# Optimization experiments

Hardware: AMD Instinct MI355X
Metric: run time of the kernel (lower is better)

Reference implementation:

```python
import jax, jax.numpy as jnp
import numpy as np
from jax import lax

V, E, H, MLP, NCLS = 50000, 100, 100, 300, 3
B, T, C = 256, 128, 255


def _lstm_dir(x, Wih, Whh, bih, bhh, reverse):
    # x: [T, B, E]; PyTorch gate order i, f, g, o
    Bsz = x.shape[1]
    h0 = jnp.zeros((Bsz, H), x.dtype)
    c0 = jnp.zeros((Bsz, H), x.dtype)

    def step(carry, xt):
        h, c = carry
        gates = xt @ Wih.T + h @ Whh.T + (bih + bhh)  # [B, 4H]
        i, f, g, o = jnp.split(gates, 4, axis=-1)
        c = jax.nn.sigmoid(f) * c + jax.nn.sigmoid(i) * jnp.tanh(g)
        h = jax.nn.sigmoid(o) * jnp.tanh(c)
        return (h, c), h

    _, hs = lax.scan(step, (h0, c0), x, reverse=reverse)
    return hs  # [T, B, H]


def setup_inputs() -> dict:
    key = jax.random.key(0)
    ks = jax.random.split(key, 16)
    s_e = 1.0 / np.sqrt(H)
    inp = {
        "x": jax.random.randint(ks[0], (B, T), 0, V),
        "paths": jax.random.randint(ks[1], (B, C, 3), 0, T),
        "emb": jax.random.normal(ks[2], (V, E), jnp.float32),
        "Wih_f": jax.random.uniform(ks[3], (4 * H, E), jnp.float32, -s_e, s_e),
        "Whh_f": jax.random.uniform(ks[4], (4 * H, H), jnp.float32, -s_e, s_e),
        "bih_f": jax.random.uniform(ks[5], (4 * H,), jnp.float32, -s_e, s_e),
        "bhh_f": jax.random.uniform(ks[6], (4 * H,), jnp.float32, -s_e, s_e),
        "Wih_b": jax.random.uniform(ks[7], (4 * H, E), jnp.float32, -s_e, s_e),
        "Whh_b": jax.random.uniform(ks[8], (4 * H, H), jnp.float32, -s_e, s_e),
        "bih_b": jax.random.uniform(ks[9], (4 * H,), jnp.float32, -s_e, s_e),
        "bhh_b": jax.random.uniform(ks[10], (4 * H,), jnp.float32, -s_e, s_e),
        "W1": jax.random.normal(ks[11], (6 * H, MLP), jnp.float32) * 0.05,
        "b1": jnp.zeros((MLP,), jnp.float32),
        "W2": jax.random.normal(ks[12], (MLP, NCLS), jnp.float32) * 0.05,
        "b2": jnp.zeros((NCLS,), jnp.float32),
    }
    return inp


def reference(x, paths, emb, Wih_f, Whh_f, bih_f, bhh_f, Wih_b, Whh_b, bih_b, bhh_b, W1, b1, W2, b2):
    # embedding lookup (dropout is eval-mode identity)
    xe = emb[x]                      # [B, T, E]
    xe = jnp.transpose(xe, (1, 0, 2))  # [T, B, E] (seq-major like packed LSTM)
    hf = _lstm_dir(xe, Wih_f, Whh_f, bih_f, bhh_f, reverse=False)
    hb = _lstm_dir(xe, Wih_b, Whh_b, bih_b, bhh_b, reverse=True)
    h = jnp.concatenate([hf, hb], axis=-1)        # [T, B, 2H]
    hbt = jnp.transpose(h, (1, 0, 2))             # [B, T, 2H]
    # gather 3 positions per configuration; index -1 -> zero vector
    idx = jnp.clip(paths, 0, T - 1)               # [B, C, 3]
    g = hbt[jnp.arange(hbt.shape[0])[:, None, None], idx]  # [B, C, 3, 2H]
    g = jnp.where((paths >= 0)[..., None], g, 0.0)
    mlp_in = g.reshape(-1, 6 * H)                 # [B*C, 600]
    hdn = jnp.tanh(mlp_in @ W1 + b1)
    return jax.nn.softmax(hdn @ W2 + b2, axis=-1)  # [B*C, 3]
```

## Files before the change

kernel.cpp:

```cpp
#include <hip/hip_runtime.h>

typedef unsigned short u16;
typedef short short8 __attribute__((ext_vector_type(8)));
typedef float f32x4 __attribute__((ext_vector_type(4)));

__device__ __forceinline__ u16 f2b(float x){
  union{float f; unsigned u;} v; v.f = x;
  unsigned r = (v.u + 0x7FFFu + ((v.u >> 16) & 1u)) >> 16;
  return (u16)r;
}
__device__ __forceinline__ float b2f(u16 h){
  union{unsigned u; float f;} v; v.u = ((unsigned)h) << 16; return v.f;
}
__device__ __forceinline__ float sigm(float x){ return 1.0f/(1.0f + __expf(-x)); }
__device__ __forceinline__ float tanh_f(float x){ return 1.0f - 2.0f/(1.0f + __expf(2.0f*x)); }

__global__ void prep_kernel(const int* __restrict__ x, const float* __restrict__ emb,
   const float* __restrict__ Wih_f, const float* __restrict__ Whh_f,
   const float* __restrict__ bih_f, const float* __restrict__ bhh_f,
   const float* __restrict__ Wih_b, const float* __restrict__ Whh_b,
   const float* __restrict__ bih_b, const float* __restrict__ bhh_b,
   const float* __restrict__ W1,
   u16* __restrict__ xe, u16* __restrict__ wc, float* __restrict__ biasC,
   float* __restrict__ whhT, u16* __restrict__ w1b, u16* __restrict__ hbt)
{
  int id = blockIdx.x*256 + threadIdx.x;
  const int N0 = 32768*128;
  const int N1 = 832*128;
  const int N2 = 800;
  const int N3 = 80000;
  const int N4 = 672*320;
  const int N5 = 32768*24;
  if (id < N0){
    int p = id >> 7, k = id & 127;
    float v = 0.f;
    if (k < 100) v = emb[x[p]*100 + k];
    xe[id] = f2b(v);
    return;
  }
  id -= N0;
  if (id < N1){
    int n = id >> 7, k = id & 127;
    float v = 0.f;
    if (k < 100){
      if (n < 400) v = Wih_f[n*100+k];
      else if (n < 800) v = Wih_b[(n-400)*100+k];
    }
    wc[id] = f2b(v);
    return;
  }
  id -= N1;
  if (id < N2){
    biasC[id] = (id < 400) ? (bih_f[id]+bhh_f[id]) : (bih_b[id-400]+bhh_b[id-400]);
    return;
  }
  id -= N2;
  if (id < N3){
    int d = id / 40000; int rem = id - d*40000; int k = rem / 400; int j = rem - k*400;
    const float* W = d ? Whh_b : Whh_f;
    whhT[id] = W[j*100 + k];
    return;
  }
  id -= N3;
  if (id < N4){
    int k = id / 320; int n = id - k*320;
    int seg = k / 224; int wwk = k - seg*224;
    float v = 0.f;
    if (n < 300 && wwk < 200) v = W1[(seg*200 + wwk)*300 + n];
    w1b[n*672 + k] = f2b(v);
    return;
  }
  id -= N4;
  if (id < N5){
    int p = id / 24; int k = id - p*24;
    hbt[p*224 + 200 + k] = 0;
  }
}

__global__ __launch_bounds__(256) void gemm1_kernel(const u16* __restrict__ xe,
    const u16* __restrict__ wc, const float* __restrict__ biasC, u16* __restrict__ inp)
{
  __shared__ __align__(16) u16 As[64*136];
  __shared__ __align__(16) u16 Bs[64*136];
  const int m0 = blockIdx.x*64, n0 = blockIdx.y*64;
  const int tid = threadIdx.x;
  #pragma unroll
  for (int i=0;i<4;i++){
    int f = i*256 + tid;
    int row = f >> 4, c8 = f & 15;
    *(uint4*)&As[row*136 + c8*8] = *(const uint4*)&xe[(m0+row)*128 + c8*8];
    *(uint4*)&Bs[row*136 + c8*8] = *(const uint4*)&wc[(n0+row)*128 + c8*8];
  }
  __syncthreads();
  const int w = tid >> 6, lane = tid & 63, col = lane & 15, quad = lane >> 4;
  f32x4 acc[4];
  #pragma unroll
  for (int nt=0;nt<4;nt++) acc[nt] = (f32x4){0.f,0.f,0.f,0.f};
  #pragma unroll
  for (int kc=0;kc<4;kc++){
    short8 af = *(const short8*)&As[(w*16+col)*136 + kc*32 + quad*8];
    #pragma unroll
    for (int nt=0;nt<4;nt++){
      short8 bfrag = *(const short8*)&Bs[(nt*16+col)*136 + kc*32 + quad*8];
      acc[nt] = __builtin_amdgcn_mfma_f32_16x16x32_bf16(af, bfrag, acc[nt], 0, 0, 0);
    }
  }
  #pragma unroll
  for (int nt=0;nt<4;nt++){
    int n = n0 + nt*16 + col;
    if (n < 800){
      float bs = biasC[n];
      int dir = (n >= 400) ? 1 : 0;
      int j = n - dir*400;
      #pragma unroll
      for (int r=0;r<4;r++){
        int m = m0 + w*16 + quad*4 + r;
        inp[(dir*32768 + m)*400 + j] = f2b(acc[nt][r] + bs);
      }
    }
  }
}

__global__ __launch_bounds__(448, 4) void lstm_kernel(const u16* __restrict__ inp,
    const float* __restrict__ whhT, u16* __restrict__ hbt)
{
  const int cid = blockIdx.x;
  const int b = cid & 255, dir = cid >> 8;
  const int jj = threadIdx.x;
  __shared__ __align__(16) float hs[104];
  __shared__ float act[400];
  float whh[100];
  if (jj < 400){
    const float* wp = whhT + dir*40000 + jj;
    #pragma unroll
    for (int k=0;k<100;k++) whh[k] = wp[k*400];
  }
  if (jj < 104) hs[jj] = 0.f;
  float c = 0.f;
  const u16* ip = inp + (dir*32768 + b*128)*400;
  u16* hp = hbt + b*128*224;
  __syncthreads();
  for (int step=0; step<128; step++){
    int t = dir ? (127-step) : step;
    if (jj < 400){
      float pre = b2f(ip[t*400 + jj]);
      const float4* h4 = (const float4*)hs;
      float a0=0.f,a1=0.f,a2=0.f,a3=0.f;
      #pragma unroll
      for (int kk=0;kk<25;kk++){
        float4 hv = h4[kk];
        a0 = fmaf(whh[4*kk+0], hv.x, a0);
        a1 = fmaf(whh[4*kk+1], hv.y, a1);
        a2 = fmaf(whh[4*kk+2], hv.z, a2);
        a3 = fmaf(whh[4*kk+3], hv.w, a3);
      }
      float xg = pre + ((a0+a1)+(a2+a3));
      act[jj] = (jj >= 200 && jj < 300) ? tanh_f(xg) : sigm(xg);
    }
    __syncthreads();
    if (jj < 100){
      float ig = act[jj], fg = act[100+jj], gg = act[200+jj], og = act[300+jj];
      c = fg*c + ig*gg;
      float hk = og * tanh_f(c);
      hs[jj] = hk;
      hp[t*224 + dir*100 + jj] = f2b(hk);
    }
    __syncthreads();
  }
}

__global__ __launch_bounds__(512) void mlp_kernel(const u16* __restrict__ hbt,
    const u16* __restrict__ w1b, const int* __restrict__ paths,
    const float* __restrict__ b1, const float* __restrict__ W2,
    const float* __restrict__ b2, float* __restrict__ out)
{
  __shared__ __align__(16) u16 As[128*40];
  __shared__ __align__(16) u16 Bs[320*40];
  const int m0 = blockIdx.x*128;
  const int tid = threadIdx.x;
  const int arow = tid >> 2, ac8 = tid & 3;
  const int am = m0 + arow;
  const int ab = am / 255;
  const int w = tid >> 6, lane = tid & 63, col = lane & 15, quad = lane >> 4;
  f32x4 acc[20];
  #pragma unroll
  for (int nt=0;nt<20;nt++) acc[nt] = (f32x4){0.f,0.f,0.f,0.f};
  for (int kc=0;kc<21;kc++){
    __syncthreads();
    for (int f = tid; f < 1280; f += 512){
      int br = f >> 2, bc = f & 3;
      *(uint4*)&Bs[br*40 + bc*8] = *(const uint4*)&w1b[br*672 + kc*32 + bc*8];
    }
    int seg = (kc >= 14) ? 2 : (kc >= 7 ? 1 : 0);
    int ko = kc - seg*7;
    int it = paths[am*3 + seg];
    uint4 v = make_uint4(0u,0u,0u,0u);
    if (it >= 0){
      int t = it > 127 ? 127 : it;
      v = *(const uint4*)&hbt[(ab*128 + t)*224 + ko*32 + ac8*8];
    }
    *(uint4*)&As[arow*40 + ac8*8] = v;
    __syncthreads();
    short8 af = *(const short8*)&As[(w*16+col)*40 + quad*8];
    #pragma unroll
    for (int nt=0;nt<20;nt++){
      short8 bfrag = *(const short8*)&Bs[(nt*16+col)*40 + quad*8];
      acc[nt] = __builtin_amdgcn_mfma_f32_16x16x32_bf16(af, bfrag, acc[nt], 0, 0, 0);
    }
  }
  float pz[4][3];
  #pragma unroll
  for (int r=0;r<4;r++){ pz[r][0]=0.f; pz[r][1]=0.f; pz[r][2]=0.f; }
  #pragma unroll
  for (int nt=0;nt<20;nt++){
    int n = nt*16 + col;
    if (n < 300){
      float bb = b1[n];
      float w20 = W2[n*3+0], w21 = W2[n*3+1], w22 = W2[n*3+2];
      #pragma unroll
      for (int r=0;r<4;r++){
        float hdn = tanh_f(acc[nt][r] + bb);
        pz[r][0] = fmaf(hdn, w20, pz[r][0]);
        pz[r][1] = fmaf(hdn, w21, pz[r][1]);
        pz[r][2] = fmaf(hdn, w22, pz[r][2]);
      }
    }
  }
  #pragma unroll
  for (int off=1; off<16; off<<=1){
    #pragma unroll
    for (int r=0;r<4;r++){
      pz[r][0] += __shfl_xor(pz[r][0], off, 64);
      pz[r][1] += __shfl_xor(pz[r][1], off, 64);
      pz[r][2] += __shfl_xor(pz[r][2], off, 64);
    }
  }
  float c0 = b2[0], c1 = b2[1], c2 = b2[2];
  #pragma unroll
  for (int r=0;r<4;r++){
    float z0 = pz[r][0]+c0, z1 = pz[r][1]+c1, z2 = pz[r][2]+c2;
    float mx = fmaxf(z0, fmaxf(z1, z2));
    float e0 = __expf(z0-mx), e1 = __expf(z1-mx), e2 = __expf(z2-mx);
    float inv = 1.0f/(e0+e1+e2);
    if (col < 3){
      float pv = (col==0 ? e0 : (col==1 ? e1 : e2)) * inv;
      out[(m0 + w*16 + quad*4 + r)*3 + col] = pv;
    }
  }
}

extern "C" void kernel_launch(void* const* d_in, const int* in_sizes, int n_in,
                              void* d_out, int out_size, void* d_ws, size_t ws_size,
                              hipStream_t stream)
{
  const int*   x     = (const int*)  d_in[0];
  const int*   paths = (const int*)  d_in[1];
  const float* emb   = (const float*)d_in[2];
  const float* Wih_f = (const float*)d_in[3];
  const float* Whh_f = (const float*)d_in[4];
  const float* bih_f = (const float*)d_in[5];
  const float* bhh_f = (const float*)d_in[6];
  const float* Wih_b = (const float*)d_in[7];
  const float* Whh_b = (const float*)d_in[8];
  const float* bih_b = (const float*)d_in[9];
  const float* bhh_b = (const float*)d_in[10];
  const float* W1    = (const float*)d_in[11];
  const float* b1    = (const float*)d_in[12];
  const float* W2    = (const float*)d_in[13];
  const float* b2    = (const float*)d_in[14];
  float* out = (float*)d_out;

  char* ws = (char*)d_ws;
  u16*   xe    = (u16*)  (ws + 0);
  u16*   wc    = (u16*)  (ws + 8388608);
  float* biasC = (float*)(ws + 8601600);
  float* whhT  = (float*)(ws + 8604800);
  u16*   w1b   = (u16*)  (ws + 8924800);
  u16*   inp   = (u16*)  (ws + 9354880);
  u16*   hbt   = (u16*)  (ws + 61783680);

  const int prep_total = 32768*128 + 832*128 + 800 + 80000 + 672*320 + 32768*24;
  prep_kernel<<<(prep_total + 255)/256, 256, 0, stream>>>(
      x, emb, Wih_f, Whh_f, bih_f, bhh_f, Wih_b, Whh_b, bih_b, bhh_b, W1,
      xe, wc, biasC, whhT, w1b, hbt);
  gemm1_kernel<<<dim3(512, 13), 256, 0, stream>>>(xe, wc, biasC, inp);
  lstm_kernel<<<512, 448, 0, stream>>>(inp, whhT, hbt);
  mlp_kernel<<<510, 512, 0, stream>>>(hbt, w1b, paths, b1, W2, b2, out);
}
```

Before: 364.4 us.

## Split LSTM recurrent dot product across two threads per gate

The recurrent matvec in the LSTM kernel now uses two threads per gate row. Each thread holds 50 weights instead of 100, and the two halves are combined with a lane shuffle. The Whh weights are repacked into an interleaved layout to match, and the per-step pointer arithmetic for t is replaced with incrementing pointers. This halves the serial FMA chain per step on the latency-bound recurrence and lowers register pressure. In exchange the block grows to 832 threads, each step adds a shuffle, and only half the threads do the activation.

```diff
diff --git a/kernel.cpp b/kernel.cpp
--- a/kernel.cpp
+++ b/kernel.cpp
@@ -22,7 +22,7 @@
    const float* __restrict__ bih_b, const float* __restrict__ bhh_b,
    const float* __restrict__ W1,
    u16* __restrict__ xe, u16* __restrict__ wc, float* __restrict__ biasC,
-   float* __restrict__ whhT, u16* __restrict__ w1b, u16* __restrict__ hbt)
+   float* __restrict__ whhP, u16* __restrict__ w1b, u16* __restrict__ hbt)
 {
   int id = blockIdx.x*256 + threadIdx.x;
   const int N0 = 32768*128;
@@ -56,9 +56,10 @@
   }
   id -= N2;
   if (id < N3){
-    int d = id / 40000; int rem = id - d*40000; int k = rem / 400; int j = rem - k*400;
+    int d = id / 40000; int rem = id - d*40000; int kk = rem / 800; int p = rem - kk*800;
+    int j = p >> 1, half = p & 1;
     const float* W = d ? Whh_b : Whh_f;
-    whhT[id] = W[j*100 + k];
+    whhP[id] = W[j*100 + half*50 + kk];
     return;
   }
   id -= N3;
@@ -121,50 +122,60 @@
   }
 }
 
-__global__ __launch_bounds__(448, 4) void lstm_kernel(const u16* __restrict__ inp,
-    const float* __restrict__ whhT, u16* __restrict__ hbt)
+__global__ __launch_bounds__(832, 7) void lstm_kernel(const u16* __restrict__ inp,
+    const float* __restrict__ whhP, u16* __restrict__ hbt)
 {
   const int cid = blockIdx.x;
   const int b = cid & 255, dir = cid >> 8;
-  const int jj = threadIdx.x;
+  const int tid = threadIdx.x;
+  const int j = tid >> 1, half = tid & 1;
   __shared__ __align__(16) float hs[104];
   __shared__ float act[400];
-  float whh[100];
-  if (jj < 400){
-    const float* wp = whhT + dir*40000 + jj;
+  float whh[50];
+  if (tid < 800){
+    const float* wp = whhP + dir*40000 + tid;
     #pragma unroll
-    for (int k=0;k<100;k++) whh[k] = wp[k*400];
-  }
-  if (jj < 104) hs[jj] = 0.f;
+    for (int k=0;k<50;k++) whh[k] = wp[k*800];
+  }
+  if (tid < 104) hs[tid] = 0.f;
   float c = 0.f;
-  const u16* ip = inp + (dir*32768 + b*128)*400;
-  u16* hp = hbt + b*128*224;
+  const u16* ipt = inp + (dir*32768 + b*128)*400 + (dir ? 127*400 : 0);
+  u16* hpt = hbt + b*128*224 + (dir ? 127*224 : 0) + dir*100 + tid;
+  const int dIp = dir ? -400 : 400;
+  const int dHp = dir ? -224 : 224;
   __syncthreads();
   for (int step=0; step<128; step++){
-    int t = dir ? (127-step) : step;
-    if (jj < 400){
-      float pre = b2f(ip[t*400 + jj]);
-      const float4* h4 = (const float4*)hs;
+    if (tid < 800){
+      const float2* h2 = (const float2*)(hs + half*50);
       float a0=0.f,a1=0.f,a2=0.f,a3=0.f;
       #pragma unroll
-      for (int kk=0;kk<25;kk++){
-        float4 hv = h4[kk];
-        a0 = fmaf(whh[4*kk+0], hv.x, a0);
-        a1 = fmaf(whh[4*kk+1], hv.y, a1);
-        a2 = fmaf(whh[4*kk+2], hv.z, a2);
-        a3 = fmaf(whh[4*kk+3], hv.w, a3);
+      for (int kk=0;kk<12;kk++){
+        float2 u = h2[2*kk], v = h2[2*kk+1];
+        a0 = fmaf(whh[4*kk+0], u.x, a0);
+        a1 = fmaf(whh[4*kk+1], u.y, a1);
+        a2 = fmaf(whh[4*kk+2], v.x, a2);
+        a3 = fmaf(whh[4*kk+3], v.y, a3);
       }
-      float xg = pre + ((a0+a1)+(a2+a3));
-      act[jj] = (jj >= 200 && jj < 300) ? tanh_f(xg) : sigm(xg);
+      { float2 u = h2[24];
+        a0 = fmaf(whh[48], u.x, a0);
+        a1 = fmaf(whh[49], u.y, a1); }
+      float part = (a0+a2)+(a1+a3);
+      part += __shfl_xor(part, 1, 64);
+      if (half == 0){
+        float xg = b2f(ipt[j]) + part;
+        act[j] = (j >= 200 && j < 300) ? tanh_f(xg) : sigm(xg);
+      }
     }
     __syncthreads();
-    if (jj < 100){
-      float ig = act[jj], fg = act[100+jj], gg = act[200+jj], og = act[300+jj];
+    if (tid < 100){
+      float ig = act[tid], fg = act[100+tid], gg = act[200+tid], og = act[300+tid];
       c = fg*c + ig*gg;
       float hk = og * tanh_f(c);
-      hs[jj] = hk;
-      hp[t*224 + dir*100 + jj] = f2b(hk);
-    }
+      hs[tid] = hk;
+      *hpt = f2b(hk);
+      hpt += dHp;
+    }
+    ipt += dIp;
     __syncthreads();
   }
 }
@@ -274,7 +285,7 @@
   u16*   xe    = (u16*)  (ws + 0);
   u16*   wc    = (u16*)  (ws + 8388608);
   float* biasC = (float*)(ws + 8601600);
-  float* whhT  = (float*)(ws + 8604800);
+  float* whhP  = (float*)(ws + 8604800);
   u16*   w1b   = (u16*)  (ws + 8924800);
   u16*   inp   = (u16*)  (ws + 9354880);
   u16*   hbt   = (u16*)  (ws + 61783680);
@@ -282,8 +293,8 @@
   const int prep_total = 32768*128 + 832*128 + 800 + 80000 + 672*320 + 32768*24;
   prep_kernel<<<(prep_total + 255)/256, 256, 0, stream>>>(
       x, emb, Wih_f, Whh_f, bih_f, bhh_f, Wih_b, Whh_b, bih_b, bhh_b, W1,
-      xe, wc, biasC, whhT, w1b, hbt);
+      xe, wc, biasC, whhP, w1b, hbt);
   gemm1_kernel<<<dim3(512, 13), 256, 0, stream>>>(xe, wc, biasC, inp);
-  lstm_kernel<<<512, 448, 0, stream>>>(inp, whhT, hbt);
+  lstm_kernel<<<512, 832, 0, stream>>>(inp, whhP, hbt);
   mlp_kernel<<<510, 512, 0, stream>>>(hbt, w1b, paths, b1, W2, b2, out);
 }
```

After: 529.0 us. 1.45x slower.

## Move LSTM recurrence to bf16 MFMA with split hi/lo precision, batching 8 sequences per block

Applied to the files above, without the earlier changes.

The recurrent h@Whh product moves from per-thread fp32 FMA over register-held weights to bf16 MFMA instructions. Weights and hidden state are each split into hi and lo bf16 parts (three MFMAs per chunk) to keep close to fp32 accuracy. Each block now handles 8 batch sequences of one direction (64 blocks instead of 512), and a dedicated warp prefetches the next step's input gates into double-buffered LDS. The prep kernel is reworked to emit the weights in MFMA fragment layout. The aim is more work per recurrent step and less per-step serial latency, at the cost of using only 64 blocks and relying on the split-bf16 scheme for accuracy.

```diff
diff --git a/kernel.cpp b/kernel.cpp
--- a/kernel.cpp
+++ b/kernel.cpp
@@ -22,13 +22,13 @@
    const float* __restrict__ bih_b, const float* __restrict__ bhh_b,
    const float* __restrict__ W1,
    u16* __restrict__ xe, u16* __restrict__ wc, float* __restrict__ biasC,
-   float* __restrict__ whhT, u16* __restrict__ w1b, u16* __restrict__ hbt)
+   u16* __restrict__ whhF, u16* __restrict__ w1b, u16* __restrict__ hbt)
 {
   int id = blockIdx.x*256 + threadIdx.x;
   const int N0 = 32768*128;
   const int N1 = 832*128;
   const int N2 = 800;
-  const int N3 = 80000;
+  const int N3 = 229376;
   const int N4 = 672*320;
   const int N5 = 32768*24;
   if (id < N0){
@@ -56,9 +56,24 @@
   }
   id -= N2;
   if (id < N3){
-    int d = id / 40000; int rem = id - d*40000; int k = rem / 400; int j = rem - k*400;
-    const float* W = d ? Whh_b : Whh_f;
-    whhT[id] = W[j*100 + k];
+    int dir = id / 114688; int r = id - dir*114688;
+    int tau = r >> 12;
+    int r2 = r & 4095;
+    int kc = r2 >> 10; int r3 = r2 & 1023;
+    int s  = r3 >> 9;  int r4 = r3 & 511;
+    int l  = r4 >> 3;  int e  = r4 & 7;
+    int g  = tau / 7;
+    int j  = (tau - g*7)*16 + (l & 15);
+    int kk = kc*32 + (l >> 4)*8 + e;
+    float v = 0.f;
+    if (j < 100 && kk < 100){
+      const float* W = dir ? Whh_b : Whh_f;
+      v = W[(g*100 + j)*100 + kk];
+    }
+    u16 hi = f2b(v);
+    u16 outv = hi;
+    if (s){ float lor = v - b2f(hi); outv = f2b(lor); }
+    whhF[id] = outv;
     return;
   }
   id -= N3;
@@ -121,49 +136,113 @@
   }
 }
 
-__global__ __launch_bounds__(448, 4) void lstm_kernel(const u16* __restrict__ inp,
-    const float* __restrict__ whhT, u16* __restrict__ hbt)
-{
-  const int cid = blockIdx.x;
-  const int b = cid & 255, dir = cid >> 8;
-  const int jj = threadIdx.x;
-  __shared__ __align__(16) float hs[104];
-  __shared__ float act[400];
-  float whh[100];
-  if (jj < 400){
-    const float* wp = whhT + dir*40000 + jj;
-    #pragma unroll
-    for (int k=0;k<100;k++) whh[k] = wp[k*400];
-  }
-  if (jj < 104) hs[jj] = 0.f;
-  float c = 0.f;
-  const u16* ip = inp + (dir*32768 + b*128)*400;
-  u16* hp = hbt + b*128*224;
+__global__ __launch_bounds__(512, 2) void lstm_kernel(const u16* __restrict__ inp,
+    const u16* __restrict__ whhF, u16* __restrict__ hbt)
+{
+  __shared__ __align__(16) u16 hhk[2][2][16][16][8];
+  __shared__ __align__(16) u16 inp_s[2][8][400];
+  const int beta = blockIdx.x;
+  const int dir = beta >> 5, b0 = (beta & 31) * 8;
+  const int tid = threadIdx.x;
+  const int w = tid >> 6, lane = tid & 63, col = lane & 15, q = lane >> 4;
+
+  for (int i = tid; i < 1024; i += 512) ((uint4*)hhk)[i] = make_uint4(0u,0u,0u,0u);
+
+  short8 wf[4][4][2];
+  f32x4 acc[4];
+  float cst[2]; cst[0] = 0.f; cst[1] = 0.f;
+  if (w < 7){
+    const u16* wp = whhF + (size_t)dir*114688;
+    #pragma unroll
+    for (int gi=0; gi<4; gi++)
+      #pragma unroll
+      for (int kc=0; kc<4; kc++)
+        #pragma unroll
+        for (int s=0; s<2; s++)
+          wf[gi][kc][s] = *(const short8*)&wp[(7*gi + w)*4096 + kc*1024 + s*512 + lane*8];
+  }
+  if (w == 7){
+    const int t0 = dir ? 127 : 0;
+    #pragma unroll
+    for (int i=0;i<7;i++){
+      int v = i*64 + lane;
+      if (v < 400){
+        int ch = v/50, off = v - ch*50;
+        const u16* gp = inp + ((size_t)(dir*32768 + (b0+ch)*128 + t0))*400 + off*8;
+        *(uint4*)&inp_s[0][ch][off*8] = *(const uint4*)gp;
+      }
+    }
+  }
   __syncthreads();
+
+  const int jl = 16*w + col;
+  const bool jv = (w < 7) && (jl < 100);
+  const int qq = q & 1;
+
   for (int step=0; step<128; step++){
-    int t = dir ? (127-step) : step;
-    if (jj < 400){
-      float pre = b2f(ip[t*400 + jj]);
-      const float4* h4 = (const float4*)hs;
-      float a0=0.f,a1=0.f,a2=0.f,a3=0.f;
-      #pragma unroll
-      for (int kk=0;kk<25;kk++){
-        float4 hv = h4[kk];
-        a0 = fmaf(whh[4*kk+0], hv.x, a0);
-        a1 = fmaf(whh[4*kk+1], hv.y, a1);
-        a2 = fmaf(whh[4*kk+2], hv.z, a2);
-        a3 = fmaf(whh[4*kk+3], hv.w, a3);
-      }
-      float xg = pre + ((a0+a1)+(a2+a3));
-      act[jj] = (jj >= 200 && jj < 300) ? tanh_f(xg) : sigm(xg);
-    }
-    __syncthreads();
-    if (jj < 100){
-      float ig = act[jj], fg = act[100+jj], gg = act[200+jj], og = act[300+jj];
-      c = fg*c + ig*gg;
-      float hk = og * tanh_f(c);
-      hs[jj] = hk;
-      hp[t*224 + dir*100 + jj] = f2b(hk);
+    const int t = dir ? 127-step : step;
+    const int par = step & 1;
+    if (w < 7){
+      short8 ah[4], al[4];
+      #pragma unroll
+      for (int kc=0; kc<4; kc++){
+        ah[kc] = *(const short8*)&hhk[par][0][kc*4+q][col][0];
+        al[kc] = *(const short8*)&hhk[par][1][kc*4+q][col][0];
+      }
+      #pragma unroll
+      for (int gi=0; gi<4; gi++){
+        f32x4 a = (f32x4){0.f,0.f,0.f,0.f};
+        #pragma unroll
+        for (int kc=0; kc<4; kc++){
+          a = __builtin_amdgcn_mfma_f32_16x16x32_bf16(ah[kc], wf[gi][kc][0], a, 0, 0, 0);
+          a = __builtin_amdgcn_mfma_f32_16x16x32_bf16(al[kc], wf[gi][kc][0], a, 0, 0, 0);
+          a = __builtin_amdgcn_mfma_f32_16x16x32_bf16(ah[kc], wf[gi][kc][1], a, 0, 0, 0);
+        }
+        acc[gi] = a;
+      }
+    }
+    if (w == 7 && step < 127){
+      int tn = dir ? 127-(step+1) : step+1;
+      #pragma unroll
+      for (int i=0;i<7;i++){
+        int v = i*64 + lane;
+        if (v < 400){
+          int ch = v/50, off = v - ch*50;
+          const u16* gp = inp + ((size_t)(dir*32768 + (b0+ch)*128 + tn))*400 + off*8;
+          *(uint4*)&inp_s[(step+1)&1][ch][off*8] = *(const uint4*)gp;
+        }
+      }
+    }
+    if (w < 7){
+      #pragma unroll
+      for (int u=0; u<2; u++){
+        float p0 = __shfl(acc[0][2+u], (lane+32)&63);
+        float p1 = __shfl(acc[1][2+u], (lane+32)&63);
+        float p2 = __shfl(acc[2][2+u], (lane+32)&63);
+        float p3 = __shfl(acc[3][2+u], (lane+32)&63);
+        float gI = (q < 2) ? acc[0][u] : p0;
+        float gF = (q < 2) ? acc[1][u] : p1;
+        float gG = (q < 2) ? acc[2][u] : p2;
+        float gO = (q < 2) ? acc[3][u] : p3;
+        if (jv){
+          int rr = (q >> 1)*2 + u;
+          int ch = qq*4 + rr;
+          const u16* ip = &inp_s[par][ch][0];
+          gI += b2f(ip[jl]);
+          gF += b2f(ip[100+jl]);
+          gG += b2f(ip[200+jl]);
+          gO += b2f(ip[300+jl]);
+          float cc = sigm(gF)*cst[u] + sigm(gI)*tanh_f(gG);
+          cst[u] = cc;
+          float h = sigm(gO)*tanh_f(cc);
+          u16 hi = f2b(h);
+          float lor = h - b2f(hi);
+          u16 lo = f2b(lor);
+          hhk[par^1][0][jl>>3][ch][jl&7] = hi;
+          hhk[par^1][1][jl>>3][ch][jl&7] = lo;
+          hbt[((size_t)(b0+ch)*128 + t)*224 + dir*100 + jl] = hi;
+        }
+      }
     }
     __syncthreads();
   }
@@ -274,16 +353,16 @@
   u16*   xe    = (u16*)  (ws + 0);
   u16*   wc    = (u16*)  (ws + 8388608);
   float* biasC = (float*)(ws + 8601600);
-  float* whhT  = (float*)(ws + 8604800);
-  u16*   w1b   = (u16*)  (ws + 8924800);
-  u16*   inp   = (u16*)  (ws + 9354880);
-  u16*   hbt   = (u16*)  (ws + 61783680);
-
-  const int prep_total = 32768*128 + 832*128 + 800 + 80000 + 672*320 + 32768*24;
+  u16*   whhF  = (u16*)  (ws + 8604800);
+  u16*   w1b   = (u16*)  (ws + 9063552);
+  u16*   inp   = (u16*)  (ws + 9493632);
+  u16*   hbt   = (u16*)  (ws + 61922432);
+
+  const int prep_total = 32768*128 + 832*128 + 800 + 229376 + 672*320 + 32768*24;
   prep_kernel<<<(prep_total + 255)/256, 256, 0, stream>>>(
       x, emb, Wih_f, Whh_f, bih_f, bhh_f, Wih_b, Whh_b, bih_b, bhh_b, W1,
-      xe, wc, biasC, whhT, w1b, hbt);
+      xe, wc, biasC, whhF, w1b, hbt);
   gemm1_kernel<<<dim3(512, 13), 256, 0, stream>>>(xe, wc, biasC, inp);
-  lstm_kernel<<<512, 448, 0, stream>>>(inp, whhT, hbt);
+  lstm_kernel<<<64, 512, 0, stream>>>(inp, whhF, hbt);
   mlp_kernel<<<510, 512, 0, stream>>>(hbt, w1b, paths, b1, W2, b2, out);
 }
```

After: 420.5 us. 1.15x slower.

## Rewrite LSTM recurrence in inline asm with gate-interleaved layout and lane swizzles

Applied to the files above, without the earlier changes.

Reorders the Whh rows and the precomputed input gates so the four gates of each hidden unit sit in adjacent lanes. The recurrent step then exchanges gate values with ds_swizzle inside a wavefront instead of going through shared memory plus an extra barrier. The step is hand-written in inline assembly with pipelined LDS reads, double-buffered hidden state and a single barrier per timestep. This targets the per-step latency of the serial recurrence. In exchange it adds fragile hand-scheduled register use (about 140 VGPRs) and drops the occupancy hint from launch_bounds.

```diff
diff --git a/kernel.cpp b/kernel.cpp
--- a/kernel.cpp
+++ b/kernel.cpp
@@ -22,7 +22,7 @@
    const float* __restrict__ bih_b, const float* __restrict__ bhh_b,
    const float* __restrict__ W1,
    u16* __restrict__ xe, u16* __restrict__ wc, float* __restrict__ biasC,
-   float* __restrict__ whhT, u16* __restrict__ w1b, u16* __restrict__ hbt)
+   float* __restrict__ whhR, u16* __restrict__ w1b, u16* __restrict__ hbt)
 {
   int id = blockIdx.x*256 + threadIdx.x;
   const int N0 = 32768*128;
@@ -56,9 +56,10 @@
   }
   id -= N2;
   if (id < N3){
-    int d = id / 40000; int rem = id - d*40000; int k = rem / 400; int j = rem - k*400;
+    int d = id / 40000; int rem = id - d*40000; int p = rem / 100; int k = rem - p*100;
+    int uu = p >> 2, gg = p & 3;
     const float* W = d ? Whh_b : Whh_f;
-    whhT[id] = W[j*100 + k];
+    whhR[id] = W[(gg*100 + uu)*100 + k];
     return;
   }
   id -= N3;
@@ -112,60 +113,209 @@
       float bs = biasC[n];
       int dir = (n >= 400) ? 1 : 0;
       int j = n - dir*400;
+      int gg = j / 100, uu = j - gg*100;
+      int pj = uu*4 + gg;
       #pragma unroll
       for (int r=0;r<4;r++){
         int m = m0 + w*16 + quad*4 + r;
-        inp[(dir*32768 + m)*400 + j] = f2b(acc[nt][r] + bs);
+        inp[(dir*32768 + m)*400 + pj] = f2b(acc[nt][r] + bs);
       }
     }
   }
 }
 
-__global__ __launch_bounds__(448, 4) void lstm_kernel(const u16* __restrict__ inp,
-    const float* __restrict__ whhT, u16* __restrict__ hbt)
+#define DG(W0,W1,W2,W3,S0,S1,S2,S3,OFF) \
+  "s_waitcnt lgkmcnt(3)\n\t" \
+  "v_fmac_f32 v16, v" #W0 ", v" #S0 "\n\t" \
+  "v_fmac_f32 v17, v" #W1 ", v" #S1 "\n\t" \
+  "v_fmac_f32 v18, v" #W2 ", v" #S2 "\n\t" \
+  "v_fmac_f32 v19, v" #W3 ", v" #S3 "\n\t" \
+  "ds_read_b128 v[" #S0 ":" #S3 "], v30 offset:" #OFF "\n\t"
+#define DGT(W0,W1,W2,W3,S0,S1,S2,S3,CNT) \
+  "s_waitcnt lgkmcnt(" #CNT ")\n\t" \
+  "v_fmac_f32 v16, v" #W0 ", v" #S0 "\n\t" \
+  "v_fmac_f32 v17, v" #W1 ", v" #S1 "\n\t" \
+  "v_fmac_f32 v18, v" #W2 ", v" #S2 "\n\t" \
+  "v_fmac_f32 v19, v" #W3 ", v" #S3 "\n\t"
+
+__global__ __launch_bounds__(448) void lstm_kernel(const u16* __restrict__ inp,
+    const float* __restrict__ whhR, u16* __restrict__ hbt)
 {
+  __shared__ __align__(16) float hs2[2][128];
   const int cid = blockIdx.x;
   const int b = cid & 255, dir = cid >> 8;
-  const int jj = threadIdx.x;
-  __shared__ __align__(16) float hs[104];
-  __shared__ float act[400];
-  float whh[100];
-  if (jj < 400){
-    const float* wp = whhT + dir*40000 + jj;
-    #pragma unroll
-    for (int k=0;k<100;k++) whh[k] = wp[k*400];
-  }
-  if (jj < 104) hs[jj] = 0.f;
-  float c = 0.f;
-  const u16* ip = inp + (dir*32768 + b*128)*400;
-  u16* hp = hbt + b*128*224;
+  const int tid = threadIdx.x;
+  for (int i = tid; i < 256; i += 448) ((float*)hs2)[i] = 0.f;
   __syncthreads();
-  for (int step=0; step<128; step++){
-    int t = dir ? (127-step) : step;
-    if (jj < 400){
-      float pre = b2f(ip[t*400 + jj]);
-      const float4* h4 = (const float4*)hs;
-      float a0=0.f,a1=0.f,a2=0.f,a3=0.f;
-      #pragma unroll
-      for (int kk=0;kk<25;kk++){
-        float4 hv = h4[kk];
-        a0 = fmaf(whh[4*kk+0], hv.x, a0);
-        a1 = fmaf(whh[4*kk+1], hv.y, a1);
-        a2 = fmaf(whh[4*kk+2], hv.z, a2);
-        a3 = fmaf(whh[4*kk+3], hv.w, a3);
-      }
-      float xg = pre + ((a0+a1)+(a2+a3));
-      act[jj] = (jj >= 200 && jj < 300) ? tanh_f(xg) : sigm(xg);
-    }
-    __syncthreads();
-    if (jj < 100){
-      float ig = act[jj], fg = act[100+jj], gg = act[200+jj], og = act[300+jj];
-      c = fg*c + ig*gg;
-      float hk = og * tanh_f(c);
-      hs[jj] = hk;
-      hp[t*224 + dir*100 + jj] = f2b(hk);
-    }
-    __syncthreads();
+  if (tid < 400){
+    const int u = tid >> 2, g = tid & 3;
+    unsigned long long fe  = __ballot(1);
+    unsigned long long g0e = __ballot(g == 0);
+    unsigned long long g1e = __ballot(g == 1);
+    unsigned long long g1m = __ballot((g & 1) != 0);
+    unsigned long long g2m = __ballot((g & 2) != 0);
+    const int t0 = dir ? 127 : 0;
+    const int dIb = dir ? -800 : 800;
+    const int dHb = dir ? -448 : 448;
+    unsigned ra = (unsigned)(size_t)&hs2[0][0];
+    unsigned ha = ra + 512u + 4u*(unsigned)u;
+    unsigned wo = (unsigned)(dir*40000 + tid*100) * 4u;
+    unsigned io = (unsigned)((dir*32768 + b*128 + t0)*400 + tid) * 2u;
+    unsigned ho = (unsigned)((b*128 + t0)*224 + dir*100 + u) * 2u;
+    asm volatile(
+      "v_mov_b32 v30, %[ra]\n\t"
+      "v_mov_b32 v31, %[ha]\n\t"
+      "v_mov_b32 v32, %[ho]\n\t"
+      "v_mov_b32 v33, %[io]\n\t"
+      "v_mov_b32 v38, 0\n\t"
+      "s_mov_b32 s20, 128\n\t"
+      "global_load_ushort v37, v33, %[ib]\n\t"
+      "v_add_u32 v33, %[dis], v33\n\t"
+      "global_load_dwordx4 v[40:43],   %[wo], %[wb]\n\t"
+      "global_load_dwordx4 v[44:47],   %[wo], %[wb] offset:16\n\t"
+      "global_load_dwordx4 v[48:51],   %[wo], %[wb] offset:32\n\t"
+      "global_load_dwordx4 v[52:55],   %[wo], %[wb] offset:48\n\t"
+      "global_load_dwordx4 v[56:59],   %[wo], %[wb] offset:64\n\t"
+      "global_load_dwordx4 v[60:63],   %[wo], %[wb] offset:80\n\t"
+      "global_load_dwordx4 v[64:67],   %[wo], %[wb] offset:96\n\t"
+      "global_load_dwordx4 v[68:71],   %[wo], %[wb] offset:112\n\t"
+      "global_load_dwordx4 v[72:75],   %[wo], %[wb] offset:128\n\t"
+      "global_load_dwordx4 v[76:79],   %[wo], %[wb] offset:144\n\t"
+      "global_load_dwordx4 v[80:83],   %[wo], %[wb] offset:160\n\t"
+      "global_load_dwordx4 v[84:87],   %[wo], %[wb] offset:176\n\t"
+      "global_load_dwordx4 v[88:91],   %[wo], %[wb] offset:192\n\t"
+      "global_load_dwordx4 v[92:95],   %[wo], %[wb] offset:208\n\t"
+      "global_load_dwordx4 v[96:99],   %[wo], %[wb] offset:224\n\t"
+      "global_load_dwordx4 v[100:103], %[wo], %[wb] offset:240\n\t"
+      "global_load_dwordx4 v[104:107], %[wo], %[wb] offset:256\n\t"
+      "global_load_dwordx4 v[108:111], %[wo], %[wb] offset:272\n\t"
+      "global_load_dwordx4 v[112:115], %[wo], %[wb] offset:288\n\t"
+      "global_load_dwordx4 v[116:119], %[wo], %[wb] offset:304\n\t"
+      "global_load_dwordx4 v[120:123], %[wo], %[wb] offset:320\n\t"
+      "global_load_dwordx4 v[124:127], %[wo], %[wb] offset:336\n\t"
+      "global_load_dwordx4 v[128:131], %[wo], %[wb] offset:352\n\t"
+      "global_load_dwordx4 v[132:135], %[wo], %[wb] offset:368\n\t"
+      "global_load_dwordx4 v[136:139], %[wo], %[wb] offset:384\n\t"
+      "s_waitcnt vmcnt(0)\n\t"
+      "LSTM_T%=:\n\t"
+      "s_waitcnt vmcnt(0)\n\t"
+      "v_mov_b32 v36, v37\n\t"
+      "global_load_ushort v37, v33, %[ib]\n\t"
+      "v_add_u32 v33, %[dis], v33\n\t"
+      "ds_read_b128 v[0:3], v30\n\t"
+      "ds_read_b128 v[4:7], v30 offset:16\n\t"
+      "ds_read_b128 v[8:11], v30 offset:32\n\t"
+      "ds_read_b128 v[12:15], v30 offset:48\n\t"
+      "v_mov_b32 v16, 0\n\t"
+      "v_mov_b32 v17, 0\n\t"
+      "v_mov_b32 v18, 0\n\t"
+      "v_mov_b32 v19, 0\n\t"
+      DG(40,41,42,43,   0,1,2,3,    64)
+      DG(44,45,46,47,   4,5,6,7,    80)
+      DG(48,49,50,51,   8,9,10,11,  96)
+      DG(52,53,54,55,   12,13,14,15,112)
+      DG(56,57,58,59,   0,1,2,3,    128)
+      DG(60,61,62,63,   4,5,6,7,    144)
+      DG(64,65,66,67,   8,9,10,11,  160)
+      DG(68,69,70,71,   12,13,14,15,176)
+      DG(72,73,74,75,   0,1,2,3,    192)
+      DG(76,77,78,79,   4,5,6,7,    208)
+      DG(80,81,82,83,   8,9,10,11,  224)
+      DG(84,85,86,87,   12,13,14,15,240)
+      DG(88,89,90,91,   0,1,2,3,    256)
+      DG(92,93,94,95,   4,5,6,7,    272)
+      DG(96,97,98,99,   8,9,10,11,  288)
+      DG(100,101,102,103, 12,13,14,15,304)
+      DG(104,105,106,107, 0,1,2,3,    320)
+      DG(108,109,110,111, 4,5,6,7,    336)
+      DG(112,113,114,115, 8,9,10,11,  352)
+      DG(116,117,118,119, 12,13,14,15,368)
+      DG(120,121,122,123, 0,1,2,3,    384)
+      DGT(124,125,126,127, 4,5,6,7,   3)
+      DGT(128,129,130,131, 8,9,10,11, 2)
+      DGT(132,133,134,135, 12,13,14,15,1)
+      DGT(136,137,138,139, 0,1,2,3,   0)
+      "v_add_f32 v16, v16, v17\n\t"
+      "v_add_f32 v18, v18, v19\n\t"
+      "v_add_f32 v16, v16, v18\n\t"
+      "v_lshlrev_b32 v24, 16, v36\n\t"
+      "v_add_f32 v16, v16, v24\n\t"
+      "ds_swizzle_b32 v25, v16 offset:0x041f\n\t"
+      "ds_swizzle_b32 v26, v16 offset:0x081f\n\t"
+      "s_waitcnt lgkmcnt(0)\n\t"
+      "ds_swizzle_b32 v27, v25 offset:0x081f\n\t"
+      "s_waitcnt lgkmcnt(0)\n\t"
+      "v_cndmask_b32 v28, v16, v25, %[g1m]\n\t"
+      "v_cndmask_b32 v29, v26, v27, %[g1m]\n\t"
+      "v_cndmask_b32 v20, v28, v29, %[g2m]\n\t"
+      "v_cndmask_b32 v22, v29, v28, %[g2m]\n\t"
+      "v_cndmask_b32 v24, v25, v16, %[g1m]\n\t"
+      "v_cndmask_b32 v25, v27, v26, %[g1m]\n\t"
+      "v_cndmask_b32 v21, v24, v25, %[g2m]\n\t"
+      "v_cndmask_b32 v23, v25, v24, %[g2m]\n\t"
+      "v_mul_f32 v24, 0xbfb8aa3b, v21\n\t"
+      "v_mul_f32 v25, 0xbfb8aa3b, v20\n\t"
+      "v_mul_f32 v26, 0x4038aa3b, v22\n\t"
+      "v_exp_f32 v24, v24\n\t"
+      "v_exp_f32 v25, v25\n\t"
+      "v_exp_f32 v26, v26\n\t"
+      "v_add_f32 v24, 1.0, v24\n\t"
+      "v_add_f32 v25, 1.0, v25\n\t"
+      "v_add_f32 v26, 1.0, v26\n\t"
+      "v_rcp_f32 v24, v24\n\t"
+      "v_rcp_f32 v25, v25\n\t"
+      "v_rcp_f32 v26, v26\n\t"
+      "v_mov_b32 v27, 1.0\n\t"
+      "v_fmac_f32 v27, -2.0, v26\n\t"
+      "v_mul_f32 v25, v25, v27\n\t"
+      "v_fmac_f32 v25, v24, v38\n\t"
+      "v_mov_b32 v38, v25\n\t"
+      "v_mul_f32 v24, 0x4038aa3b, v38\n\t"
+      "v_mul_f32 v26, 0xbfb8aa3b, v23\n\t"
+      "v_exp_f32 v24, v24\n\t"
+      "v_exp_f32 v26, v26\n\t"
+      "v_add_f32 v24, 1.0, v24\n\t"
+      "v_add_f32 v26, 1.0, v26\n\t"
+      "v_rcp_f32 v24, v24\n\t"
+      "v_rcp_f32 v26, v26\n\t"
+      "v_mov_b32 v27, 1.0\n\t"
+      "v_fmac_f32 v27, -2.0, v24\n\t"
+      "v_mul_f32 v28, v26, v27\n\t"
+      "v_cvt_pk_bf16_f32 v39, v28, v28\n\t"
+      "s_mov_b64 exec, %[g0e]\n\t"
+      "ds_write_b32 v31, v28\n\t"
+      "s_mov_b64 exec, %[g1e]\n\t"
+      "global_store_short v32, v39, %[hb]\n\t"
+      "s_mov_b64 exec, %[fe]\n\t"
+      "v_add_u32 v32, %[dhs], v32\n\t"
+      "v_xor_b32 v30, 0x200, v30\n\t"
+      "v_xor_b32 v31, 0x200, v31\n\t"
+      "s_waitcnt lgkmcnt(0)\n\t"
+      "s_barrier\n\t"
+      "s_sub_u32 s20, s20, 1\n\t"
+      "s_cmp_lg_u32 s20, 0\n\t"
+      "s_cbranch_scc1 LSTM_T%=\n\t"
+      :
+      : [ra]"v"(ra), [ha]"v"(ha), [ho]"v"(ho), [io]"v"(io), [wo]"v"(wo),
+        [wb]"s"(whhR), [ib]"s"(inp), [hb]"s"(hbt),
+        [dis]"s"(dIb), [dhs]"s"(dHb),
+        [fe]"s"(fe), [g0e]"s"(g0e), [g1e]"s"(g1e), [g1m]"s"(g1m), [g2m]"s"(g2m)
+      : "memory","scc","s20","s21",
+        "v0","v1","v2","v3","v4","v5","v6","v7","v8","v9",
+        "v10","v11","v12","v13","v14","v15","v16","v17","v18","v19",
+        "v20","v21","v22","v23","v24","v25","v26","v27","v28","v29",
+        "v30","v31","v32","v33","v34","v35","v36","v37","v38","v39",
+        "v40","v41","v42","v43","v44","v45","v46","v47","v48","v49",
+        "v50","v51","v52","v53","v54","v55","v56","v57","v58","v59",
+        "v60","v61","v62","v63","v64","v65","v66","v67","v68","v69",
+        "v70","v71","v72","v73","v74","v75","v76","v77","v78","v79",
+        "v80","v81","v82","v83","v84","v85","v86","v87","v88","v89",
+        "v90","v91","v92","v93","v94","v95","v96","v97","v98","v99",
+        "v100","v101","v102","v103","v104","v105","v106","v107","v108","v109",
+        "v110","v111","v112","v113","v114","v115","v116","v117","v118","v119",
+        "v120","v121","v122","v123","v124","v125","v126","v127","v128","v129",
+        "v130","v131","v132","v133","v134","v135","v136","v137","v138","v139"
+    );
   }
 }
 
@@ -274,7 +424,7 @@
   u16*   xe    = (u16*)  (ws + 0);
   u16*   wc    = (u16*)  (ws + 8388608);
   float* biasC = (float*)(ws + 8601600);
-  float* whhT  = (float*)(ws + 8604800);
+  float* whhR  = (float*)(ws + 8604800);
   u16*   w1b   = (u16*)  (ws + 8924800);
   u16*   inp   = (u16*)  (ws + 9354880);
   u16*   hbt   = (u16*)  (ws + 61783680);
@@ -282,8 +432,8 @@
   const int prep_total = 32768*128 + 832*128 + 800 + 80000 + 672*320 + 32768*24;
   prep_kernel<<<(prep_total + 255)/256, 256, 0, stream>>>(
       x, emb, Wih_f, Whh_f, bih_f, bhh_f, Wih_b, Whh_b, bih_b, bhh_b, W1,
-      xe, wc, biasC, whhT, w1b, hbt);
+      xe, wc, biasC, whhR, w1b, hbt);
   gemm1_kernel<<<dim3(512, 13), 256, 0, stream>>>(xe, wc, biasC, inp);
-  lstm_kernel<<<512, 448, 0, stream>>>(inp, whhT, hbt);
+  lstm_kernel<<<512, 448, 0, stream>>>(inp, whhR, hbt);
   mlp_kernel<<<510, 512, 0, stream>>>(hbt, w1b, paths, b1, W2, b2, out);
 }
```

New measurement: 418.1 us. 1.15x slower.
